# Performance work log

Measured on AMD Instinct MI355X. Metric: run time of the kernel, lower is better.

Reference implementation:

```python
import jax, jax.numpy as jnp
import numpy as np

N = 50000
E = 800000
IN_F = 256
ATT_D = 256
H = 8
D_K = ATT_D // H  # 32
NORM_IDX = 0  # opt['attention_norm_idx']


def setup_inputs() -> dict:
    key = jax.random.key(0)
    ks = jax.random.split(key, 10)
    x = jax.random.normal(ks[0], (N, IN_F), dtype=jnp.float32)
    edge = jax.random.randint(ks[1], (2, E), 0, N, dtype=jnp.int64)
    edge_weights = jax.random.uniform(ks[2], (E,), dtype=jnp.float32)
    s = 0.02
    Wq = jax.random.normal(ks[3], (ATT_D, IN_F), dtype=jnp.float32) * s
    bq = jax.random.normal(ks[4], (ATT_D,), dtype=jnp.float32) * s
    Wk = jax.random.normal(ks[5], (ATT_D, IN_F), dtype=jnp.float32) * s
    bk = jax.random.normal(ks[6], (ATT_D,), dtype=jnp.float32) * s
    Wv = jax.random.normal(ks[7], (ATT_D, IN_F), dtype=jnp.float32) * s
    bv = jax.random.normal(ks[8], (ATT_D,), dtype=jnp.float32) * s
    return {"x": x, "edge": edge, "edge_weights": edge_weights,
            "Wq": Wq, "bq": bq, "Wk": Wk, "bk": bk, "Wv": Wv, "bv": bv}


def _segment_softmax(logits, seg, num_segments):
    # scatter-softmax grouped by seg (torch_geometric.utils.softmax semantics)
    m = jax.ops.segment_max(logits, seg, num_segments=num_segments)  # [N, H]
    ex = jnp.exp(logits - m[seg])
    s = jax.ops.segment_sum(ex, seg, num_segments=num_segments)
    return ex / (s[seg] + 1e-16)


def reference(x, edge, edge_weights, Wq, bq, Wk, bk, Wv, bv):
    # Linear projections, then [N, H, D_K] -> transpose to [N, D_K, H]
    q = (x @ Wq.T + bq).reshape(N, H, D_K).transpose(0, 2, 1)
    k = (x @ Wk.T + bk).reshape(N, H, D_K).transpose(0, 2, 1)
    v = (x @ Wv.T + bv).reshape(N, H, D_K).transpose(0, 2, 1)
    src = q[edge[0]]      # [E, D_K, H]
    dst_k = k[edge[1]]    # [E, D_K, H]
    prods = jnp.sum(src * dst_k, axis=1) / np.sqrt(D_K)  # [E, H]
    prods = prods * edge_weights[:, None]
    attention = _segment_softmax(prods, edge[NORM_IDX], N)  # [E, H]
    return attention, v
```

## Files before the change

### kernel.cpp

```cpp
#include <hip/hip_runtime.h>

#define NN 50000
#define EE 800000
#define FF 256
#define HH 8
#define DK 32

typedef short bf16x8 __attribute__((ext_vector_type(8)));
typedef float f32x4  __attribute__((ext_vector_type(4)));

__device__ __forceinline__ float b2f(short s) {
    return __uint_as_float(((unsigned)(unsigned short)s) << 16);
}
__device__ __forceinline__ short f2b(float f) {
    unsigned u = __float_as_uint(f);
    return (short)((u + 0x7fff + ((u >> 16) & 1)) >> 16);
}

__device__ __forceinline__ void gld16(void* lds, const void* g) {
    __builtin_amdgcn_global_load_lds(
        (const __attribute__((address_space(1))) unsigned int*)g,
        (__attribute__((address_space(3))) unsigned int*)lds,
        16, 0, 0);
}

__device__ __forceinline__ int xcd_swz(int bid, int nwg) {
    int q = nwg >> 3, r = nwg & 7, x = bid & 7, i = bid >> 3;
    int base = x < r ? x * (q + 1) : r * (q + 1) + (x - r) * q;
    return base + i;
}

__global__ __launch_bounds__(256) void sniff_all(
    const void* x, const void* ew, const void* wq, const void* bq,
    const void* wk, const void* bk, const void* wv, const void* bv,
    const void* edge, int* __restrict__ flags)
{
    __shared__ int tot;
    if (threadIdx.x == 0) tot = 0;
    __syncthreads();
    int b = blockIdx.x;
    if (b < 8) {
        const void* ptrs[8] = {x, ew, wq, bq, wk, bk, wv, bv};
        const int   ns[8]   = {NN * FF, EE, FF * FF, FF, FF * FF, FF, FF * FF, FF};
        const unsigned short* p = (const unsigned short*)ptrs[b];
        int half = ns[b] >> 1;
        int S = half < 4096 ? half : 4096;
        int cnt = 0;
        for (int i = threadIdx.x; i < S; i += 256) {
            unsigned v = p[2 * i];
            cnt += (((v >> 7) & 0xFF) >= 0xC0) ? 1 : 0;
        }
        atomicAdd(&tot, cnt);
        __syncthreads();
        if (threadIdx.x == 0) flags[b] = (tot * 32 > S) ? 1 : 0;
    } else {
        const unsigned* e32 = (const unsigned*)edge;
        int cnt = 0;
        for (int i = threadIdx.x; i < 4096; i += 256)
            cnt += (e32[2 * i + 1] != 0u) ? 1 : 0;
        atomicAdd(&tot, cnt);
        __syncthreads();
        if (threadIdx.x == 0) flags[8] = (tot < 100) ? 1 : 0;
    }
}

__global__ __launch_bounds__(256) void x_to_bf16(
    const void* __restrict__ x, short* __restrict__ xb,
    const int* __restrict__ flags)
{
    int i = blockIdx.x * 256 + threadIdx.x;
    int base = i * 8;
    bf16x8 v;
    if (flags[0]) {
        const f32x4* p = (const f32x4*)((const float*)x + base);
        f32x4 a = p[0], c = p[1];
        #pragma unroll
        for (int j = 0; j < 4; ++j) { v[j] = f2b(a[j]); v[4 + j] = f2b(c[j]); }
    } else {
        v = *(const bf16x8*)((const short*)x + base);
    }
    *(bf16x8*)(xb + base) = v;
}

__global__ __launch_bounds__(256) void convert_wb(
    const void* wq, const void* wk, const void* wv,
    const void* bq, const void* bk, const void* bv,
    short* __restrict__ wb, float* __restrict__ bb,
    const int* __restrict__ flags)
{
    int b = blockIdx.x;
    if (b < 96) {
        int mat = b >> 5;
        const void* src = mat == 0 ? wq : mat == 1 ? wk : wv;
        int isf = flags[2 + mat * 2];
        int base = (b & 31) * 2048 + threadIdx.x * 8;
        bf16x8 v;
        if (isf) {
            const f32x4* pp = (const f32x4*)((const float*)src + base);
            f32x4 a = pp[0], c = pp[1];
            #pragma unroll
            for (int j = 0; j < 4; ++j) { v[j] = f2b(a[j]); v[4 + j] = f2b(c[j]); }
        } else {
            v = *(const bf16x8*)((const short*)src + base);
        }
        int row = base >> 8, k = base & 255;
        int s = k >> 5, quad = (k >> 3) & 3;
        int pc = (row << 2) + (quad ^ ((row >> 1) & 3));
        *(bf16x8*)(wb + mat * (FF * FF) + s * 8192 + pc * 8) = v;
    } else {
        #pragma unroll
        for (int mat = 0; mat < 3; ++mat) {
            const void* src = mat == 0 ? bq : mat == 1 ? bk : bv;
            int isf = flags[3 + mat * 2];
            int i = threadIdx.x;
            bb[mat * FF + i] = isf ? ((const float*)src)[i]
                                   : b2f(((const short*)src)[i]);
        }
    }
}

__global__ __launch_bounds__(128, 2) void qkv_gemm(
    const void* __restrict__ x, const short* __restrict__ xbp,
    const short* __restrict__ wb, const float* __restrict__ bb,
    short* __restrict__ qo, short* __restrict__ ko, float* __restrict__ vo,
    const int* __restrict__ flags, int matbase, int nmats, int use_xb)
{
    __shared__ __align__(16) short wlds[2][8192];
    const int isf32x = flags[0];
    const int tid = threadIdx.x, wave = tid >> 6, lane = tid & 63;
    const int l16 = lane & 15, quad = lane >> 4;

    const int nwg = 782 * nmats;
    const int w = xcd_swz(blockIdx.x, nwg);
    const int xbk = w / nmats;
    const int mat = matbase + (w - xbk * nmats);

    const short* W = wb + mat * (FF * FF);
    const int rows0 = xbk * 64 + wave * 32;

    const int rdo = l16 * 32 + ((quad ^ ((l16 >> 1) & 3)) << 3);
    const int koff = quad * 8;

    bf16x8 afrag[2][8];
    #pragma unroll
    for (int rg = 0; rg < 2; ++rg) {
        const int rowa = rows0 + rg * 16 + l16;
        const int rowc = rowa < NN ? rowa : NN - 1;
        const size_t xrow = (size_t)rowc * FF;
        if (use_xb) {
            const short* xp = xbp + xrow + koff;
            #pragma unroll
            for (int s = 0; s < 8; ++s)
                afrag[rg][s] = *(const bf16x8*)(xp + s * 32);
        } else if (isf32x) {
            #pragma unroll
            for (int s = 0; s < 8; ++s) {
                const f32x4* p = (const f32x4*)((const float*)x + xrow + s * 32 + koff);
                f32x4 u = p[0], v2 = p[1];
                #pragma unroll
                for (int j = 0; j < 4; ++j) {
                    afrag[rg][s][j]     = f2b(u[j]);
                    afrag[rg][s][4 + j] = f2b(v2[j]);
                }
            }
        } else {
            #pragma unroll
            for (int s = 0; s < 8; ++s)
                afrag[rg][s] = *(const bf16x8*)((const short*)x + xrow + s * 32 + koff);
        }
    }

    #define STAGE(buf, s) do {                                                  \
        const short* gs_ = W + (s) * 8192;                                      \
        _Pragma("unroll")                                                       \
        for (int i_ = 0; i_ < 8; ++i_)                                          \
            gld16(&wlds[buf][(i_ * 128 + (tid & ~63)) * 8],                     \
                  gs_ + (size_t)(i_ * 128 + tid) * 8);                          \
    } while (0)

    STAGE(0, 0);
    __syncthreads();

    f32x4 acc[2][16] = {};
    #pragma unroll
    for (int s = 0; s < 8; ++s) {
        const int cur = s & 1;
        if (s < 7) STAGE(cur ^ 1, s + 1);
        const short* ws0 = &wlds[cur][rdo];
        #pragma unroll
        for (int c = 0; c < 16; ++c) {
            bf16x8 bf = *(const bf16x8*)(ws0 + c * 512);
            acc[0][c] = __builtin_amdgcn_mfma_f32_16x16x32_bf16(afrag[0][s], bf, acc[0][c], 0, 0, 0);
            acc[1][c] = __builtin_amdgcn_mfma_f32_16x16x32_bf16(afrag[1][s], bf, acc[1][c], 0, 0, 0);
        }
        __syncthreads();
    }
    #undef STAGE

    const float* bias = bb + mat * FF;
    short* slice = (short*)wlds + wave * 8192;

    if (mat == 2) {
        float* lsf = (float*)slice;
        #pragma unroll
        for (int h = 0; h < 2; ++h) {
            #pragma unroll
            for (int rg = 0; rg < 2; ++rg)
                #pragma unroll
                for (int ci = 0; ci < 8; ++ci) {
                    int c = ci * 2 + h;
                    int col = c * 16 + l16;
                    float bv = bias[col];
                    int pcl = l16 * 8 + ci;
                    #pragma unroll
                    for (int rr = 0; rr < 4; ++rr)
                        lsf[(rg * 16 + quad * 4 + rr) * 128 + pcl] = acc[rg][c][rr] + bv;
                }
            #pragma unroll
            for (int it = 0; it < 16; ++it) {
                int idx = it * 64 + lane;
                int r = idx >> 5, cc = idx & 31;
                int row = rows0 + r;
                if (row < NN)
                    *(f32x4*)(vo + (size_t)row * FF + h * 128 + cc * 4) =
                        ((const f32x4*)lsf)[idx];
            }
        }
    } else {
        #pragma unroll
        for (int rg = 0; rg < 2; ++rg)
            #pragma unroll
            for (int c = 0; c < 16; ++c) {
                int col = c * 16 + l16;
                float bv = bias[col];
                #pragma unroll
                for (int rr = 0; rr < 4; ++rr)
                    slice[(rg * 16 + quad * 4 + rr) * 256 + col] = f2b(acc[rg][c][rr] + bv);
            }
        short* out = (mat == 0) ? qo : ko;
        #pragma unroll
        for (int it = 0; it < 16; ++it) {
            int idx = it * 64 + lane;
            int r = idx >> 5, cc = idx & 31;
            int row = rows0 + r;
            if (row < NN)
                *(bf16x8*)(out + (size_t)row * FF + cc * 8) =
                    *(const bf16x8*)(slice + r * 256 + cc * 8);
        }
    }
}

__device__ __forceinline__ float edge_exp_f(
    const int* __restrict__ edge, const void* __restrict__ ew,
    const short* __restrict__ q, const short* __restrict__ k,
    int t, int isf32, int is64, int* s_out)
{
    int e = t >> 3, h = t & 7;
    int s = is64 ? edge[2 * (size_t)e] : edge[e];
    int d = is64 ? edge[2 * ((size_t)EE + e)] : edge[EE + e];
    *s_out = s;
    const short* qp = q + (size_t)s * FF + h * DK;
    const short* kp = k + (size_t)d * FF + h * DK;
    float dot = 0.f;
    #pragma unroll
    for (int i = 0; i < 4; ++i) {
        bf16x8 qa = *(const bf16x8*)(qp + i * 8);
        bf16x8 ka = *(const bf16x8*)(kp + i * 8);
        #pragma unroll
        for (int j = 0; j < 8; ++j) dot += b2f(qa[j]) * b2f(ka[j]);
    }
    float w = isf32 ? ((const float*)ew)[e] : b2f(((const short*)ew)[e]);
    return __expf(dot * 0.17677669529663687f * w);
}

__global__ __launch_bounds__(256) void edge_pass_a(
    const int* __restrict__ edge, const void* __restrict__ ew,
    const short* __restrict__ q, const short* __restrict__ k,
    float* __restrict__ sums, float* __restrict__ expbuf,
    const int* __restrict__ flags)
{
    int t = blockIdx.x * 256 + threadIdx.x;
    int s;
    float exv = edge_exp_f(edge, ew, q, k, t, flags[1], flags[8], &s);
    expbuf[t] = exv;
    atomicAdd(&sums[s * HH + (threadIdx.x & 7)], exv);
}

__global__ __launch_bounds__(256) void rsum_inv(float* __restrict__ sums)
{
    int i = blockIdx.x * 256 + threadIdx.x;
    if (i < NN * HH) sums[i] = 1.0f / (sums[i] + 1e-16f);
}

__global__ __launch_bounds__(256) void edge_pass_b(
    const int* __restrict__ edge, const float* __restrict__ sums,
    const float* __restrict__ expbuf, float* __restrict__ att,
    const int* __restrict__ flags)
{
    int t = blockIdx.x * 256 + threadIdx.x;
    int e = t >> 3;
    int s = flags[8] ? edge[2 * (size_t)e] : edge[e];
    att[t] = expbuf[t] * sums[s * HH + (t & 7)];
}

extern "C" void kernel_launch(void* const* d_in, const int* in_sizes, int n_in,
                              void* d_out, int out_size, void* d_ws, size_t ws_size,
                              hipStream_t stream) {
    const void* x    = d_in[0];
    const int*  edge = (const int*)d_in[1];
    const void* ew   = d_in[2];
    const void* Wq   = d_in[3];
    const void* bq   = d_in[4];
    const void* Wk   = d_in[5];
    const void* bk   = d_in[6];
    const void* Wv   = d_in[7];
    const void* bv   = d_in[8];

    float* att_out = (float*)d_out;
    float* v_out   = att_out + (size_t)EE * HH;

    char*  ws    = (char*)d_ws;
    int*   flags = (int*)ws;
    float* sums  = (float*)(ws + 256);
    const size_t SUMS_B = (size_t)NN * HH * 4;
    const size_t Q_B    = (size_t)NN * FF * 2;
    const size_t XB_B   = (size_t)NN * FF * 2;
    short* q_  = (short*)(ws + 256 + SUMS_B);
    short* wb  = (short*)(ws + 256 + SUMS_B + Q_B);
    float* bb  = (float*)(ws + 256 + SUMS_B + Q_B + 3 * FF * FF * 2);
    const size_t BASE_B = 256 + SUMS_B + Q_B + 3 * FF * FF * 2 + 3 * FF * 4;
    const int xb_in_ws = (ws_size >= BASE_B + XB_B) ? 1 : 0;

    short* xb = xb_in_ws ? (short*)(ws + BASE_B) : (short*)att_out;

    short* k_   = (short*)v_out;
    float* expb = v_out + (size_t)EE * HH;

    sniff_all<<<9, 256, 0, stream>>>(x, ew, Wq, bq, Wk, bk, Wv, bv, edge, flags);
    convert_wb<<<97, 256, 0, stream>>>(Wq, Wk, Wv, bq, bk, bv, wb, bb, flags);
    x_to_bf16<<<NN * FF / 8 / 256, 256, 0, stream>>>(x, xb, flags);
    hipMemsetAsync(sums, 0, SUMS_B, stream);

    const int nEH = EE * HH;

    qkv_gemm<<<782 * 2, 128, 0, stream>>>(x, xb, wb, bb, q_, k_, nullptr,
                                          flags, 0, 2, 1);
    edge_pass_a<<<nEH / 256, 256, 0, stream>>>(edge, ew, q_, k_, sums, expb, flags);
    rsum_inv<<<(NN * HH + 255) / 256, 256, 0, stream>>>(sums);
    edge_pass_b<<<nEH / 256, 256, 0, stream>>>(edge, sums, expb, att_out, flags);
    qkv_gemm<<<782, 128, 0, stream>>>(x, xb, wb, bb, nullptr, nullptr, v_out,
                                      flags, 2, 1, xb_in_ws);
}
```

Baseline: 313.0 us.

## Drop LDS staging in QKV GEMM; read weights and store outputs directly

Removes the double-buffered global-to-LDS staging of the weight tiles in the QKV projection GEMM. MFMA B fragments are now loaded straight from global memory, relying on L2/L1 caching, and the per-stage __syncthreads barriers are gone. The LDS-based epilogue that transposed accumulators for vectorized row stores is also removed, so results are written with per-element scalar stores. This frees LDS and barriers for occupancy, but trades them for uncoalesced narrow stores and higher-latency global weight loads.

```diff
diff --git a/kernel.cpp b/kernel.cpp
--- a/kernel.cpp
+++ b/kernel.cpp
@@ -15,13 +15,6 @@
 __device__ __forceinline__ short f2b(float f) {
     unsigned u = __float_as_uint(f);
     return (short)((u + 0x7fff + ((u >> 16) & 1)) >> 16);
-}
-
-__device__ __forceinline__ void gld16(void* lds, const void* g) {
-    __builtin_amdgcn_global_load_lds(
-        (const __attribute__((address_space(1))) unsigned int*)g,
-        (__attribute__((address_space(3))) unsigned int*)lds,
-        16, 0, 0);
 }
 
 __device__ __forceinline__ int xcd_swz(int bid, int nwg) {
@@ -125,7 +118,6 @@
     short* __restrict__ qo, short* __restrict__ ko, float* __restrict__ vo,
     const int* __restrict__ flags, int matbase, int nmats, int use_xb)
 {
-    __shared__ __align__(16) short wlds[2][8192];
     const int isf32x = flags[0];
     const int tid = threadIdx.x, wave = tid >> 6, lane = tid & 63;
     const int l16 = lane & 15, quad = lane >> 4;
@@ -170,82 +162,48 @@
         }
     }
 
-    #define STAGE(buf, s) do {                                                  \
-        const short* gs_ = W + (s) * 8192;                                      \
-        _Pragma("unroll")                                                       \
-        for (int i_ = 0; i_ < 8; ++i_)                                          \
-            gld16(&wlds[buf][(i_ * 128 + (tid & ~63)) * 8],                     \
-                  gs_ + (size_t)(i_ * 128 + tid) * 8);                          \
-    } while (0)
-
-    STAGE(0, 0);
-    __syncthreads();
-
     f32x4 acc[2][16] = {};
     #pragma unroll
     for (int s = 0; s < 8; ++s) {
-        const int cur = s & 1;
-        if (s < 7) STAGE(cur ^ 1, s + 1);
-        const short* ws0 = &wlds[cur][rdo];
+        const short* ws0 = W + s * 8192 + rdo;
         #pragma unroll
         for (int c = 0; c < 16; ++c) {
             bf16x8 bf = *(const bf16x8*)(ws0 + c * 512);
             acc[0][c] = __builtin_amdgcn_mfma_f32_16x16x32_bf16(afrag[0][s], bf, acc[0][c], 0, 0, 0);
             acc[1][c] = __builtin_amdgcn_mfma_f32_16x16x32_bf16(afrag[1][s], bf, acc[1][c], 0, 0, 0);
         }
-        __syncthreads();
-    }
-    #undef STAGE
+    }
 
     const float* bias = bb + mat * FF;
-    short* slice = (short*)wlds + wave * 8192;
-
     if (mat == 2) {
-        float* lsf = (float*)slice;
-        #pragma unroll
-        for (int h = 0; h < 2; ++h) {
+        #pragma unroll
+        for (int c = 0; c < 16; ++c) {
+            int col = c * 16 + l16;
+            float bv = bias[col];
+            int pc = (col & 31) * 8 + (col >> 5);
             #pragma unroll
             for (int rg = 0; rg < 2; ++rg)
                 #pragma unroll
-                for (int ci = 0; ci < 8; ++ci) {
-                    int c = ci * 2 + h;
-                    int col = c * 16 + l16;
-                    float bv = bias[col];
-                    int pcl = l16 * 8 + ci;
-                    #pragma unroll
-                    for (int rr = 0; rr < 4; ++rr)
-                        lsf[(rg * 16 + quad * 4 + rr) * 128 + pcl] = acc[rg][c][rr] + bv;
+                for (int rr = 0; rr < 4; ++rr) {
+                    int row = rows0 + rg * 16 + quad * 4 + rr;
+                    if (row < NN)
+                        vo[(size_t)row * FF + pc] = acc[rg][c][rr] + bv;
                 }
-            #pragma unroll
-            for (int it = 0; it < 16; ++it) {
-                int idx = it * 64 + lane;
-                int r = idx >> 5, cc = idx & 31;
-                int row = rows0 + r;
-                if (row < NN)
-                    *(f32x4*)(vo + (size_t)row * FF + h * 128 + cc * 4) =
-                        ((const f32x4*)lsf)[idx];
-            }
         }
     } else {
-        #pragma unroll
-        for (int rg = 0; rg < 2; ++rg)
-            #pragma unroll
-            for (int c = 0; c < 16; ++c) {
-                int col = c * 16 + l16;
-                float bv = bias[col];
+        short* out = (mat == 0) ? qo : ko;
+        #pragma unroll
+        for (int c = 0; c < 16; ++c) {
+            int col = c * 16 + l16;
+            float bv = bias[col];
+            #pragma unroll
+            for (int rg = 0; rg < 2; ++rg)
                 #pragma unroll
-                for (int rr = 0; rr < 4; ++rr)
-                    slice[(rg * 16 + quad * 4 + rr) * 256 + col] = f2b(acc[rg][c][rr] + bv);
-            }
-        short* out = (mat == 0) ? qo : ko;
-        #pragma unroll
-        for (int it = 0; it < 16; ++it) {
-            int idx = it * 64 + lane;
-            int r = idx >> 5, cc = idx & 31;
-            int row = rows0 + r;
-            if (row < NN)
-                *(bf16x8*)(out + (size_t)row * FF + cc * 8) =
-                    *(const bf16x8*)(slice + r * 256 + cc * 8);
+                for (int rr = 0; rr < 4; ++rr) {
+                    int row = rows0 + rg * 16 + quad * 4 + rr;
+                    if (row < NN)
+                        out[(size_t)row * FF + col] = f2b(acc[rg][c][rr] + bv);
+                }
         }
     }
 }
```

After: 433.5 us. 1.38x slower.
